# Kernel optimization log

Hardware: AMD Instinct MI355X
Metric: run time of the kernel (lower is better)

Reference implementation:

```python
import jax, jax.numpy as jnp
import numpy as np

N_NODES = 50000
N_EDGES = 800000
N_GRAPHS = 500
IN_DIM = 128
HID = 96
OUT_DIM = 64


def _lin(k, fan_in, fan_out):
    return jax.random.normal(k, (fan_in, fan_out), jnp.float32) / np.float32(np.sqrt(fan_in))


def setup_inputs() -> dict:
    key = jax.random.key(0)
    ks = jax.random.split(key, 12)
    x = jax.random.normal(ks[0], (N_NODES, IN_DIM), jnp.float32)
    edge_index = jax.random.randint(ks[1], (2, N_EDGES), 0, N_NODES)
    batch = jnp.sort(jax.random.randint(ks[2], (N_NODES,), 0, N_GRAPHS))
    return {
        "x": x,
        "edge_index": edge_index,
        "batch": batch,
        # GCN conv weights (first: in->hid, rest: hid->hid)
        "W0": _lin(ks[3], IN_DIM, HID), "b0": jnp.zeros((HID,), jnp.float32),
        "W1": _lin(ks[4], HID, HID),    "b1": jnp.zeros((HID,), jnp.float32),
        "W2": _lin(ks[5], HID, HID),    "b2": jnp.zeros((HID,), jnp.float32),
        # jumping-knowledge 'cat' projection: 3*hid -> hid
        "Wjk": _lin(ks[6], 3 * HID, HID), "bjk": jnp.zeros((HID,), jnp.float32),
        # fc_o MLP: hid -> hid -> out
        "Wm1": _lin(ks[7], HID, HID),   "bm1": jnp.zeros((HID,), jnp.float32),
        "Wm2": _lin(ks[8], HID, OUT_DIM), "bm2": jnp.zeros((OUT_DIM,), jnp.float32),
    }


def reference(x, edge_index, batch, W0, b0, W1, b1, W2, b2, Wjk, bjk, Wm1, bm1, Wm2, bm2):
    n = x.shape[0]
    loop = jnp.arange(n, dtype=edge_index.dtype)
    src = jnp.concatenate([edge_index[0], loop])  # [E+N] with self-loops
    dst = jnp.concatenate([edge_index[1], loop])
    # symmetric GCN normalization: D^{-1/2} (A+I) D^{-1/2}
    deg = jax.ops.segment_sum(jnp.ones_like(dst, x.dtype), dst, num_segments=n)
    dinv = jax.lax.rsqrt(jnp.maximum(deg, 1.0))  # deg >= 1 with self-loops
    norm = dinv[src] * dinv[dst]  # [E+N]

    def gcn_conv(h, W, b):
        m = (h @ W)[src] * norm[:, None]                      # gather + scale
        return jax.ops.segment_sum(m, dst, num_segments=n) + b  # scatter-add

    h1 = jax.nn.relu(gcn_conv(x, W0, b0))
    h2 = jax.nn.relu(gcn_conv(h1, W1, b1))
    h3 = jax.nn.relu(gcn_conv(h2, W2, b2))
    # JK 'cat' + final linear (PyG BasicGNN lin)
    h = jnp.concatenate([h1, h2, h3], axis=-1) @ Wjk + bjk    # [N, HID]
    # global add pooling over graphs
    emb_o = jax.ops.segment_sum(h, batch, num_segments=N_GRAPHS)  # [G, HID]
    # fc_o MLP (eval: dropout/identity-batchnorm omitted)
    pred_o = jax.nn.relu(emb_o @ Wm1 + bm1) @ Wm2 + bm2       # [G, OUT]
    return pred_o
```

## Files before the change

kernel.cpp:

```cpp
#include <hip/hip_runtime.h>
#include <hip/hip_fp16.h>

#define NN 50000
#define NE 800000
#define NG 500
#define IND 128
#define HD 96
#define OD 64

#define SCAN_CHUNK 2048
#define SCAN_BLOCKS ((NN + SCAN_CHUNK - 1) / SCAN_CHUNK)


__global__ void zero_k(int* __restrict__ cnt) {
  int i = blockIdx.x * 256 + threadIdx.x;
  if (i < NN) cnt[i] = 0;
}

__global__ void hist_k(const int* __restrict__ dst, int* __restrict__ cnt,
                       int* __restrict__ rank) {
  int i0 = (blockIdx.x * 256 + threadIdx.x) * 8;
  if (i0 + 8 <= NE) {
    int4 d0 = *reinterpret_cast<const int4*>(&dst[i0]);
    int4 d1 = *reinterpret_cast<const int4*>(&dst[i0 + 4]);
    int4 r0, r1;
    r0.x = atomicAdd(&cnt[d0.x], 1);
    r0.y = atomicAdd(&cnt[d0.y], 1);
    r0.z = atomicAdd(&cnt[d0.z], 1);
    r0.w = atomicAdd(&cnt[d0.w], 1);
    r1.x = atomicAdd(&cnt[d1.x], 1);
    r1.y = atomicAdd(&cnt[d1.y], 1);
    r1.z = atomicAdd(&cnt[d1.z], 1);
    r1.w = atomicAdd(&cnt[d1.w], 1);
    *reinterpret_cast<int4*>(&rank[i0]) = r0;
    *reinterpret_cast<int4*>(&rank[i0 + 4]) = r1;
  } else {
    for (int i = i0; i < NE; i++) rank[i] = atomicAdd(&cnt[dst[i]], 1);
  }
}

__global__ void gstart_k(const int* __restrict__ batch, int* __restrict__ gstart) {
  int n = blockIdx.x * 256 + threadIdx.x;
  if (n >= NN) return;
  if (n == 0) {
    for (int g = 0; g <= batch[0]; g++) gstart[g] = 0;
    for (int g = batch[NN - 1] + 1; g <= NG; g++) gstart[g] = NN;
  } else {
    int b0 = batch[n - 1], b1 = batch[n];
    for (int g = b0 + 1; g <= b1; g++) gstart[g] = n;
  }
}

__global__ __launch_bounds__(256) void scan_part_k(const int* __restrict__ cnt,
                                                   int* __restrict__ bsum,
                                                   float* __restrict__ dinv) {
  __shared__ int ts[256];
  const int tid = threadIdx.x;
  const int base = blockIdx.x * SCAN_CHUNK + tid * 8;
  int s = 0;
#pragma unroll
  for (int j = 0; j < 8; j++) {
    int idx = base + j;
    if (idx < NN) {
      int c = cnt[idx];
      s += c;
      dinv[idx] = rsqrtf((float)(c + 1));
    }
  }
  ts[tid] = s;
  __syncthreads();
  for (int off = 128; off > 0; off >>= 1) {
    if (tid < off) ts[tid] += ts[tid + off];
    __syncthreads();
  }
  if (tid == 0) bsum[blockIdx.x] = ts[0];
}

__global__ __launch_bounds__(64) void scan_top_k(const int* __restrict__ bsum,
                                                 int* __restrict__ boff,
                                                 int* __restrict__ row_ptr) {
  int tid = threadIdx.x;
  int v = (tid < SCAN_BLOCKS) ? bsum[tid] : 0;
  for (int off = 1; off < 64; off <<= 1) {
    int u = __shfl_up(v, off);
    if (tid >= off) v += u;
  }
  if (tid < SCAN_BLOCKS) boff[tid] = v - bsum[tid];
  if (tid == 0) row_ptr[NN] = NE;
}

__global__ __launch_bounds__(256) void scan_fin_k(const int* __restrict__ cnt,
                                                  const int* __restrict__ boff,
                                                  int* __restrict__ row_ptr) {
  __shared__ int ts[256];
  const int tid = threadIdx.x;
  const int base = blockIdx.x * SCAN_CHUNK + tid * 8;
  int v[8];
  int s = 0;
#pragma unroll
  for (int j = 0; j < 8; j++) {
    int idx = base + j;
    v[j] = (idx < NN) ? cnt[idx] : 0;
    s += v[j];
  }
  ts[tid] = s;
  __syncthreads();
  for (int off = 1; off < 256; off <<= 1) {
    int t = (tid >= off) ? ts[tid - off] : 0;
    __syncthreads();
    ts[tid] += t;
    __syncthreads();
  }
  int run = ((tid == 0) ? 0 : ts[tid - 1]) + boff[blockIdx.x];
#pragma unroll
  for (int j = 0; j < 8; j++) {
    int idx = base + j;
    if (idx < NN) row_ptr[idx] = run;
    run += v[j];
  }
}

__global__ void fill_k(const int* __restrict__ src, const int* __restrict__ dst,
                       const int* __restrict__ row_ptr, const int* __restrict__ rank,
                       int* __restrict__ col) {
  int i0 = (blockIdx.x * 256 + threadIdx.x) * 8;
  if (i0 + 8 <= NE) {
    int4 d0 = *reinterpret_cast<const int4*>(&dst[i0]);
    int4 d1 = *reinterpret_cast<const int4*>(&dst[i0 + 4]);
    int4 s0 = *reinterpret_cast<const int4*>(&src[i0]);
    int4 s1 = *reinterpret_cast<const int4*>(&src[i0 + 4]);
    int4 r0 = *reinterpret_cast<const int4*>(&rank[i0]);
    int4 r1 = *reinterpret_cast<const int4*>(&rank[i0 + 4]);
    int p0 = row_ptr[d0.x], p1 = row_ptr[d0.y], p2 = row_ptr[d0.z], p3 = row_ptr[d0.w];
    int p4 = row_ptr[d1.x], p5 = row_ptr[d1.y], p6 = row_ptr[d1.z], p7 = row_ptr[d1.w];
    col[p0 + r0.x] = s0.x * (HD * 2);
    col[p1 + r0.y] = s0.y * (HD * 2);
    col[p2 + r0.z] = s0.z * (HD * 2);
    col[p3 + r0.w] = s0.w * (HD * 2);
    col[p4 + r1.x] = s1.x * (HD * 2);
    col[p5 + r1.y] = s1.y * (HD * 2);
    col[p6 + r1.z] = s1.z * (HD * 2);
    col[p7 + r1.w] = s1.w * (HD * 2);
  } else {
    for (int i = i0; i < NE; i++)
      col[row_ptr[dst[i]] + rank[i]] = src[i] * (HD * 2);
  }
}

template <int K>
__global__ __launch_bounds__(256) void gemm_scale_k(const float* __restrict__ h,
                                                    const float* __restrict__ W,
                                                    const float* __restrict__ dinv,
                                                    __half* __restrict__ g) {
  __shared__ float hsT[32][66];
  __shared__ __attribute__((aligned(16))) float ws[32][100];
  const int tid = threadIdx.x;
  const int rowg = tid >> 3;
  const int colg = tid & 7;
  const int row0 = blockIdx.x * 64;

  float acc[2][12];
#pragma unroll
  for (int i = 0; i < 2; i++)
#pragma unroll
    for (int j = 0; j < 12; j++) acc[i][j] = 0.f;

  for (int k0 = 0; k0 < K; k0 += 32) {
#pragma unroll
    for (int lin = tid; lin < 512; lin += 256) {
      int r = lin >> 3, q = lin & 7;
      int grow = row0 + r;
      float4 v = make_float4(0.f, 0.f, 0.f, 0.f);
      if (grow < NN) v = *reinterpret_cast<const float4*>(&h[(long)grow * K + k0 + 4 * q]);
      hsT[4 * q + 0][r] = v.x;
      hsT[4 * q + 1][r] = v.y;
      hsT[4 * q + 2][r] = v.z;
      hsT[4 * q + 3][r] = v.w;
    }
#pragma unroll
    for (int lin = tid; lin < 768; lin += 256) {
      int kk = lin / 24, c4 = lin - kk * 24;
      *reinterpret_cast<float4*>(&ws[kk][4 * c4]) =
          *reinterpret_cast<const float4*>(&W[(long)(k0 + kk) * HD + 4 * c4]);
    }
    __syncthreads();
#pragma unroll 8
    for (int k = 0; k < 32; k++) {
      float2 a = *reinterpret_cast<const float2*>(&hsT[k][2 * rowg]);
      float4 w0 = *reinterpret_cast<const float4*>(&ws[k][12 * colg]);
      float4 w1 = *reinterpret_cast<const float4*>(&ws[k][12 * colg + 4]);
      float4 w2 = *reinterpret_cast<const float4*>(&ws[k][12 * colg + 8]);
      float wv[12] = {w0.x, w0.y, w0.z, w0.w, w1.x, w1.y, w1.z, w1.w,
                      w2.x, w2.y, w2.z, w2.w};
      float av[2] = {a.x, a.y};
#pragma unroll
      for (int i = 0; i < 2; i++)
#pragma unroll
        for (int j = 0; j < 12; j++) acc[i][j] = fmaf(av[i], wv[j], acc[i][j]);
    }
    __syncthreads();
  }
#pragma unroll
  for (int i = 0; i < 2; i++) {
    int row = row0 + 2 * rowg + i;
    if (row < NN) {
      float dv = dinv[row];
      __half2 hh[6];
#pragma unroll
      for (int q = 0; q < 6; q++)
        hh[q] = __floats2half2_rn(acc[i][2 * q] * dv, acc[i][2 * q + 1] * dv);
      __half* go = g + (long)row * HD + 12 * colg;
      *reinterpret_cast<float2*>(go) = *reinterpret_cast<float2*>(&hh[0]);
      *reinterpret_cast<float2*>(go + 4) = *reinterpret_cast<float2*>(&hh[2]);
      *reinterpret_cast<float2*>(go + 8) = *reinterpret_cast<float2*>(&hh[4]);
    }
  }
}

__global__ __launch_bounds__(256) void gather_k(const __half* __restrict__ g,
                                                const int* __restrict__ row_ptr,
                                                const int* __restrict__ col,
                                                const float* __restrict__ dinv,
                                                const float* __restrict__ bias,
                                                float* __restrict__ hout) {
  int d = blockIdx.x * 4 + (threadIdx.x >> 6);
  int lane = threadIdx.x & 63;
  if (d >= NN) return;
  const int cl = (lane < 48) ? lane : 0;
  const char* gb = reinterpret_cast<const char*>(g);
  const __half2* gd = reinterpret_cast<const __half2*>(gb + (long)d * (HD * 2));
  float2 fs = __half22float2(gd[cl]);
  float accx = fs.x, accy = fs.y;
  int e = row_ptr[d];
  const int end = row_ptr[d + 1];
  while (e < end) {
    int cnt = end - e; if (cnt > 64) cnt = 64;
    int cid = (lane < cnt) ? col[e + lane] : 0;
    int j = 0;
    for (; j + 16 <= cnt; j += 16) {
      const __half2* p0  = reinterpret_cast<const __half2*>(gb + (long)__shfl(cid, j + 0));
      const __half2* p1  = reinterpret_cast<const __half2*>(gb + (long)__shfl(cid, j + 1));
      const __half2* p2  = reinterpret_cast<const __half2*>(gb + (long)__shfl(cid, j + 2));
      const __half2* p3  = reinterpret_cast<const __half2*>(gb + (long)__shfl(cid, j + 3));
      const __half2* p4  = reinterpret_cast<const __half2*>(gb + (long)__shfl(cid, j + 4));
      const __half2* p5  = reinterpret_cast<const __half2*>(gb + (long)__shfl(cid, j + 5));
      const __half2* p6  = reinterpret_cast<const __half2*>(gb + (long)__shfl(cid, j + 6));
      const __half2* p7  = reinterpret_cast<const __half2*>(gb + (long)__shfl(cid, j + 7));
      const __half2* p8  = reinterpret_cast<const __half2*>(gb + (long)__shfl(cid, j + 8));
      const __half2* p9  = reinterpret_cast<const __half2*>(gb + (long)__shfl(cid, j + 9));
      const __half2* p10 = reinterpret_cast<const __half2*>(gb + (long)__shfl(cid, j + 10));
      const __half2* p11 = reinterpret_cast<const __half2*>(gb + (long)__shfl(cid, j + 11));
      const __half2* p12 = reinterpret_cast<const __half2*>(gb + (long)__shfl(cid, j + 12));
      const __half2* p13 = reinterpret_cast<const __half2*>(gb + (long)__shfl(cid, j + 13));
      const __half2* p14 = reinterpret_cast<const __half2*>(gb + (long)__shfl(cid, j + 14));
      const __half2* p15 = reinterpret_cast<const __half2*>(gb + (long)__shfl(cid, j + 15));
      __half2 v0 = p0[cl],  v1 = p1[cl],  v2 = p2[cl],  v3 = p3[cl];
      __half2 v4 = p4[cl],  v5 = p5[cl],  v6 = p6[cl],  v7 = p7[cl];
      __half2 v8 = p8[cl],  v9 = p9[cl],  v10 = p10[cl], v11 = p11[cl];
      __half2 v12 = p12[cl], v13 = p13[cl], v14 = p14[cl], v15 = p15[cl];
      float2 f;
      f = __half22float2(v0);  accx += f.x; accy += f.y;
      f = __half22float2(v1);  accx += f.x; accy += f.y;
      f = __half22float2(v2);  accx += f.x; accy += f.y;
      f = __half22float2(v3);  accx += f.x; accy += f.y;
      f = __half22float2(v4);  accx += f.x; accy += f.y;
      f = __half22float2(v5);  accx += f.x; accy += f.y;
      f = __half22float2(v6);  accx += f.x; accy += f.y;
      f = __half22float2(v7);  accx += f.x; accy += f.y;
      f = __half22float2(v8);  accx += f.x; accy += f.y;
      f = __half22float2(v9);  accx += f.x; accy += f.y;
      f = __half22float2(v10); accx += f.x; accy += f.y;
      f = __half22float2(v11); accx += f.x; accy += f.y;
      f = __half22float2(v12); accx += f.x; accy += f.y;
      f = __half22float2(v13); accx += f.x; accy += f.y;
      f = __half22float2(v14); accx += f.x; accy += f.y;
      f = __half22float2(v15); accx += f.x; accy += f.y;
    }
    for (; j + 8 <= cnt; j += 8) {
      const __half2* q0 = reinterpret_cast<const __half2*>(gb + (long)__shfl(cid, j + 0));
      const __half2* q1 = reinterpret_cast<const __half2*>(gb + (long)__shfl(cid, j + 1));
      const __half2* q2 = reinterpret_cast<const __half2*>(gb + (long)__shfl(cid, j + 2));
      const __half2* q3 = reinterpret_cast<const __half2*>(gb + (long)__shfl(cid, j + 3));
      const __half2* q4 = reinterpret_cast<const __half2*>(gb + (long)__shfl(cid, j + 4));
      const __half2* q5 = reinterpret_cast<const __half2*>(gb + (long)__shfl(cid, j + 5));
      const __half2* q6 = reinterpret_cast<const __half2*>(gb + (long)__shfl(cid, j + 6));
      const __half2* q7 = reinterpret_cast<const __half2*>(gb + (long)__shfl(cid, j + 7));
      __half2 v0 = q0[cl], v1 = q1[cl], v2 = q2[cl], v3 = q3[cl];
      __half2 v4 = q4[cl], v5 = q5[cl], v6 = q6[cl], v7 = q7[cl];
      float2 f;
      f = __half22float2(v0); accx += f.x; accy += f.y;
      f = __half22float2(v1); accx += f.x; accy += f.y;
      f = __half22float2(v2); accx += f.x; accy += f.y;
      f = __half22float2(v3); accx += f.x; accy += f.y;
      f = __half22float2(v4); accx += f.x; accy += f.y;
      f = __half22float2(v5); accx += f.x; accy += f.y;
      f = __half22float2(v6); accx += f.x; accy += f.y;
      f = __half22float2(v7); accx += f.x; accy += f.y;
    }
    for (; j < cnt; j++) {
      const __half2* p = reinterpret_cast<const __half2*>(gb + (long)__shfl(cid, j));
      float2 f = __half22float2(p[cl]);
      accx += f.x; accy += f.y;
    }
    e += 64;
  }
  if (lane < 48) {
    float dv = dinv[d];
    float2 bb = *reinterpret_cast<const float2*>(&bias[2 * lane]);
    float v0 = fmaxf(fmaf(accx, dv, bb.x), 0.f);
    float v1 = fmaxf(fmaf(accy, dv, bb.y), 0.f);
    *reinterpret_cast<float2*>(&hout[(long)d * HD + 2 * lane]) = make_float2(v0, v1);
  }
}

__global__ __launch_bounds__(256) void pool3_k(const float* __restrict__ hA,
                                               const float* __restrict__ hB,
                                               const float* __restrict__ hC,
                                               const int* __restrict__ gstart,
                                               float* __restrict__ P) {
  __shared__ float red[240][12];
  const int g = blockIdx.x;
  const int t = threadIdx.x;
  const int q = t % 24, s = t / 24;
  const int n0 = gstart[g], n1 = gstart[g + 1];
  if (t < 240) {
    float4 aA = make_float4(0.f, 0.f, 0.f, 0.f), aB = aA, aC = aA;
    for (int n = n0 + s; n < n1; n += 10) {
      float4 v;
      v = *reinterpret_cast<const float4*>(&hA[(long)n * HD + 4 * q]);
      aA.x += v.x; aA.y += v.y; aA.z += v.z; aA.w += v.w;
      v = *reinterpret_cast<const float4*>(&hB[(long)n * HD + 4 * q]);
      aB.x += v.x; aB.y += v.y; aB.z += v.z; aB.w += v.w;
      v = *reinterpret_cast<const float4*>(&hC[(long)n * HD + 4 * q]);
      aC.x += v.x; aC.y += v.y; aC.z += v.z; aC.w += v.w;
    }
    red[t][0] = aA.x; red[t][1] = aA.y; red[t][2]  = aA.z; red[t][3]  = aA.w;
    red[t][4] = aB.x; red[t][5] = aB.y; red[t][6]  = aB.z; red[t][7]  = aB.w;
    red[t][8] = aC.x; red[t][9] = aC.y; red[t][10] = aC.z; red[t][11] = aC.w;
  }
  __syncthreads();
  if (t < 24) {
    float sum[12];
#pragma unroll
    for (int c = 0; c < 12; c++) sum[c] = 0.f;
    for (int ss = 0; ss < 10; ss++)
#pragma unroll
      for (int c = 0; c < 12; c++) sum[c] += red[ss * 24 + t][c];
#pragma unroll
    for (int k = 0; k < 4; k++) {
      P[0 * NG * HD + g * HD + 4 * t + k] = sum[k];
      P[1 * NG * HD + g * HD + 4 * t + k] = sum[4 + k];
      P[2 * NG * HD + g * HD + 4 * t + k] = sum[8 + k];
    }
  }
}


__global__ void emb_k(const float* __restrict__ P, const int* __restrict__ gstart,
                      const float* __restrict__ Wjk, const float* __restrict__ bjk,
                      float* __restrict__ emb) {
  int idx = blockIdx.x * 256 + threadIdx.x;
  if (idx >= NG * HD) return;
  int gr = idx / HD, c = idx - gr * HD;
  const float* p1 = P + (long)gr * HD;
  const float* p2 = p1 + (long)NG * HD;
  const float* p3 = p2 + (long)NG * HD;
  float acc = (float)(gstart[gr + 1] - gstart[gr]) * bjk[c];
  for (int k = 0; k < HD; k++) {
    acc = fmaf(p1[k], Wjk[k * HD + c], acc);
    acc = fmaf(p2[k], Wjk[(HD + k) * HD + c], acc);
    acc = fmaf(p3[k], Wjk[(2 * HD + k) * HD + c], acc);
  }
  emb[idx] = acc;
}

__global__ void mlp1_k(const float* __restrict__ emb, const float* __restrict__ W,
                       const float* __restrict__ b, float* __restrict__ hid) {
  int idx = blockIdx.x * 256 + threadIdx.x;
  if (idx >= NG * HD) return;
  int gr = idx / HD, c = idx - gr * HD;
  const float* e = emb + (long)gr * HD;
  float acc = b[c];
  for (int k = 0; k < HD; k++) acc = fmaf(e[k], W[k * HD + c], acc);
  hid[idx] = fmaxf(acc, 0.f);
}

__global__ void mlp2_k(const float* __restrict__ hid, const float* __restrict__ W,
                       const float* __restrict__ b, float* __restrict__ out) {
  int idx = blockIdx.x * 256 + threadIdx.x;
  if (idx >= NG * OD) return;
  int gr = idx / OD, c = idx - gr * OD;
  const float* h = hid + (long)gr * HD;
  float acc = b[c];
  for (int k = 0; k < HD; k++) acc = fmaf(h[k], W[k * OD + c], acc);
  out[idx] = acc;
}


extern "C" void kernel_launch(void* const* d_in, const int* in_sizes, int n_in,
                              void* d_out, int out_size, void* d_ws, size_t ws_size,
                              hipStream_t stream) {
  const float* x = (const float*)d_in[0];
  const int* ei = (const int*)d_in[1];
  const int* batch = (const int*)d_in[2];
  const float* W0 = (const float*)d_in[3];  const float* b0 = (const float*)d_in[4];
  const float* W1 = (const float*)d_in[5];  const float* b1 = (const float*)d_in[6];
  const float* W2 = (const float*)d_in[7];  const float* b2 = (const float*)d_in[8];
  const float* Wjk = (const float*)d_in[9]; const float* bjk = (const float*)d_in[10];
  const float* Wm1 = (const float*)d_in[11]; const float* bm1 = (const float*)d_in[12];
  const float* Wm2 = (const float*)d_in[13]; const float* bm2 = (const float*)d_in[14];
  const int* srcp = ei;
  const int* dstp = ei + NE;

  char* wp = (char*)d_ws;
  size_t off = 0;
  auto alloc = [&](size_t bytes) -> void* {
    void* p = wp + off;
    off += bytes;
    off = (off + 255) & ~(size_t)255;
    return p;
  };
  int* cnt    = (int*)alloc((size_t)NN * 4);
  int* rowp   = (int*)alloc((size_t)(NN + 1) * 4);
  int* rank   = (int*)alloc((size_t)NE * 4);
  int* colb   = (int*)alloc((size_t)NE * 4);
  float* dinv = (float*)alloc((size_t)NN * 4);
  int* gstart = (int*)alloc((size_t)(NG + 1) * 4);
  int* bsum   = (int*)alloc((size_t)SCAN_BLOCKS * 4);
  int* boff   = (int*)alloc((size_t)SCAN_BLOCKS * 4);
  __half* g   = (__half*)alloc((size_t)NN * HD * 2);
  float* hA   = (float*)alloc((size_t)NN * HD * 4);
  float* hB   = (float*)alloc((size_t)NN * HD * 4);
  float* hC   = (float*)alloc((size_t)NN * HD * 4);
  float* P    = (float*)alloc((size_t)3 * NG * HD * 4);
  float* emb  = (float*)alloc((size_t)NG * HD * 4);
  float* hid  = (float*)alloc((size_t)NG * HD * 4);

  zero_k<<<(NN + 255) / 256, 256, 0, stream>>>(cnt);

  const int eb8 = (NE / 8 + 255) / 256;
  hist_k<<<eb8, 256, 0, stream>>>(dstp, cnt, rank);
  gstart_k<<<(NN + 255) / 256, 256, 0, stream>>>(batch, gstart);
  scan_part_k<<<SCAN_BLOCKS, 256, 0, stream>>>(cnt, bsum, dinv);
  scan_top_k<<<1, 64, 0, stream>>>(bsum, boff, rowp);
  scan_fin_k<<<SCAN_BLOCKS, 256, 0, stream>>>(cnt, boff, rowp);
  fill_k<<<eb8, 256, 0, stream>>>(srcp, dstp, rowp, rank, colb);

  const int gemm_grid = (NN + 63) / 64;
  const int gath_grid = (NN + 3) / 4;
  gemm_scale_k<IND><<<gemm_grid, 256, 0, stream>>>(x, W0, dinv, g);
  gather_k<<<gath_grid, 256, 0, stream>>>(g, rowp, colb, dinv, b0, hA);
  gemm_scale_k<HD><<<gemm_grid, 256, 0, stream>>>(hA, W1, dinv, g);
  gather_k<<<gath_grid, 256, 0, stream>>>(g, rowp, colb, dinv, b1, hB);
  gemm_scale_k<HD><<<gemm_grid, 256, 0, stream>>>(hB, W2, dinv, g);
  gather_k<<<gath_grid, 256, 0, stream>>>(g, rowp, colb, dinv, b2, hC);

  pool3_k<<<NG, 256, 0, stream>>>(hA, hB, hC, gstart, P);

  emb_k<<<(NG * HD + 255) / 256, 256, 0, stream>>>(P, gstart, Wjk, bjk, emb);
  mlp1_k<<<(NG * HD + 255) / 256, 256, 0, stream>>>(emb, Wm1, bm1, hid);
  mlp2_k<<<(NG * OD + 255) / 256, 256, 0, stream>>>(hid, Wm2, bm2, (float*)d_out);
}
```

Measured before the change: 262.4 us.

## Store hidden activations in fp16 and gather four neighbors per wavefront step

Hidden layer outputs hA/hB/hC are now stored as fp16 instead of fp32. The next GEMM and the pooling kernel read them at half the bytes and convert to float on load. The gather kernel is restructured so each wavefront processes four neighbor rows at once, with 12 lanes per row loading 16 bytes each. The partial sums are then reduced with shuffles. This cuts activation traffic and raises bytes per load, at the cost of fp16 rounding of intermediate activations and an extra cross-lane reduction.

```diff
diff --git a/kernel.cpp b/kernel.cpp
--- a/kernel.cpp
+++ b/kernel.cpp
@@ -147,8 +147,8 @@
   }
 }
 
-template <int K>
-__global__ __launch_bounds__(256) void gemm_scale_k(const float* __restrict__ h,
+template <int K, typename T>
+__global__ __launch_bounds__(256) void gemm_scale_k(const T* __restrict__ h,
                                                     const float* __restrict__ W,
                                                     const float* __restrict__ dinv,
                                                     __half* __restrict__ g) {
@@ -166,16 +166,38 @@
     for (int j = 0; j < 12; j++) acc[i][j] = 0.f;
 
   for (int k0 = 0; k0 < K; k0 += 32) {
-#pragma unroll
-    for (int lin = tid; lin < 512; lin += 256) {
-      int r = lin >> 3, q = lin & 7;
-      int grow = row0 + r;
-      float4 v = make_float4(0.f, 0.f, 0.f, 0.f);
-      if (grow < NN) v = *reinterpret_cast<const float4*>(&h[(long)grow * K + k0 + 4 * q]);
-      hsT[4 * q + 0][r] = v.x;
-      hsT[4 * q + 1][r] = v.y;
-      hsT[4 * q + 2][r] = v.z;
-      hsT[4 * q + 3][r] = v.w;
+    if constexpr (sizeof(T) == 4) {
+#pragma unroll
+      for (int lin = tid; lin < 512; lin += 256) {
+        int r = lin >> 3, q = lin & 7;
+        int grow = row0 + r;
+        float4 v = make_float4(0.f, 0.f, 0.f, 0.f);
+        if (grow < NN)
+          v = *reinterpret_cast<const float4*>(&h[(long)grow * K + k0 + 4 * q]);
+        hsT[4 * q + 0][r] = v.x;
+        hsT[4 * q + 1][r] = v.y;
+        hsT[4 * q + 2][r] = v.z;
+        hsT[4 * q + 3][r] = v.w;
+      }
+    } else {
+      {
+        int r = tid >> 2, q = tid & 3;
+        int grow = row0 + r;
+        if (grow < NN) {
+          int4 raw = *reinterpret_cast<const int4*>(
+              reinterpret_cast<const __half*>(h) + (long)grow * K + k0 + 8 * q);
+          const __half2* hp = reinterpret_cast<const __half2*>(&raw);
+#pragma unroll
+          for (int t = 0; t < 4; t++) {
+            float2 f = __half22float2(hp[t]);
+            hsT[8 * q + 2 * t + 0][r] = f.x;
+            hsT[8 * q + 2 * t + 1][r] = f.y;
+          }
+        } else {
+#pragma unroll
+          for (int t = 0; t < 8; t++) hsT[8 * q + t][r] = 0.f;
+        }
+      }
     }
 #pragma unroll
     for (int lin = tid; lin < 768; lin += 256) {
@@ -222,100 +244,102 @@
                                                 const int* __restrict__ col,
                                                 const float* __restrict__ dinv,
                                                 const float* __restrict__ bias,
-                                                float* __restrict__ hout) {
+                                                __half* __restrict__ hout) {
   int d = blockIdx.x * 4 + (threadIdx.x >> 6);
   int lane = threadIdx.x & 63;
   if (d >= NN) return;
-  const int cl = (lane < 48) ? lane : 0;
+  const bool active = (lane < 48);
+  const int s = active ? (lane / 12) : 0;
+  const int c = active ? (lane % 12) : 0;
+  const int cofs = 16 * c;
   const char* gb = reinterpret_cast<const char*>(g);
-  const __half2* gd = reinterpret_cast<const __half2*>(gb + (long)d * (HD * 2));
-  float2 fs = __half22float2(gd[cl]);
-  float accx = fs.x, accy = fs.y;
+  const int own = d * (HD * 2);
+
+  float acc[8];
+#pragma unroll
+  for (int k = 0; k < 8; k++) acc[k] = 0.f;
+
+  {
+    float4 raw = *reinterpret_cast<const float4*>(gb + own + cofs);
+    const __half2* hp = reinterpret_cast<const __half2*>(&raw);
+    float m = (active && s == 0) ? 1.f : 0.f;
+#pragma unroll
+    for (int q = 0; q < 4; q++) {
+      float2 f = __half22float2(hp[q]);
+      acc[2 * q + 0] = fmaf(m, f.x, acc[2 * q + 0]);
+      acc[2 * q + 1] = fmaf(m, f.y, acc[2 * q + 1]);
+    }
+  }
+
   int e = row_ptr[d];
   const int end = row_ptr[d + 1];
   while (e < end) {
     int cnt = end - e; if (cnt > 64) cnt = 64;
-    int cid = (lane < cnt) ? col[e + lane] : 0;
+    int cid = (lane < cnt) ? col[e + lane] : own;
     int j = 0;
     for (; j + 16 <= cnt; j += 16) {
-      const __half2* p0  = reinterpret_cast<const __half2*>(gb + (long)__shfl(cid, j + 0));
-      const __half2* p1  = reinterpret_cast<const __half2*>(gb + (long)__shfl(cid, j + 1));
-      const __half2* p2  = reinterpret_cast<const __half2*>(gb + (long)__shfl(cid, j + 2));
-      const __half2* p3  = reinterpret_cast<const __half2*>(gb + (long)__shfl(cid, j + 3));
-      const __half2* p4  = reinterpret_cast<const __half2*>(gb + (long)__shfl(cid, j + 4));
-      const __half2* p5  = reinterpret_cast<const __half2*>(gb + (long)__shfl(cid, j + 5));
-      const __half2* p6  = reinterpret_cast<const __half2*>(gb + (long)__shfl(cid, j + 6));
-      const __half2* p7  = reinterpret_cast<const __half2*>(gb + (long)__shfl(cid, j + 7));
-      const __half2* p8  = reinterpret_cast<const __half2*>(gb + (long)__shfl(cid, j + 8));
-      const __half2* p9  = reinterpret_cast<const __half2*>(gb + (long)__shfl(cid, j + 9));
-      const __half2* p10 = reinterpret_cast<const __half2*>(gb + (long)__shfl(cid, j + 10));
-      const __half2* p11 = reinterpret_cast<const __half2*>(gb + (long)__shfl(cid, j + 11));
-      const __half2* p12 = reinterpret_cast<const __half2*>(gb + (long)__shfl(cid, j + 12));
-      const __half2* p13 = reinterpret_cast<const __half2*>(gb + (long)__shfl(cid, j + 13));
-      const __half2* p14 = reinterpret_cast<const __half2*>(gb + (long)__shfl(cid, j + 14));
-      const __half2* p15 = reinterpret_cast<const __half2*>(gb + (long)__shfl(cid, j + 15));
-      __half2 v0 = p0[cl],  v1 = p1[cl],  v2 = p2[cl],  v3 = p3[cl];
-      __half2 v4 = p4[cl],  v5 = p5[cl],  v6 = p6[cl],  v7 = p7[cl];
-      __half2 v8 = p8[cl],  v9 = p9[cl],  v10 = p10[cl], v11 = p11[cl];
-      __half2 v12 = p12[cl], v13 = p13[cl], v14 = p14[cl], v15 = p15[cl];
-      float2 f;
-      f = __half22float2(v0);  accx += f.x; accy += f.y;
-      f = __half22float2(v1);  accx += f.x; accy += f.y;
-      f = __half22float2(v2);  accx += f.x; accy += f.y;
-      f = __half22float2(v3);  accx += f.x; accy += f.y;
-      f = __half22float2(v4);  accx += f.x; accy += f.y;
-      f = __half22float2(v5);  accx += f.x; accy += f.y;
-      f = __half22float2(v6);  accx += f.x; accy += f.y;
-      f = __half22float2(v7);  accx += f.x; accy += f.y;
-      f = __half22float2(v8);  accx += f.x; accy += f.y;
-      f = __half22float2(v9);  accx += f.x; accy += f.y;
-      f = __half22float2(v10); accx += f.x; accy += f.y;
-      f = __half22float2(v11); accx += f.x; accy += f.y;
-      f = __half22float2(v12); accx += f.x; accy += f.y;
-      f = __half22float2(v13); accx += f.x; accy += f.y;
-      f = __half22float2(v14); accx += f.x; accy += f.y;
-      f = __half22float2(v15); accx += f.x; accy += f.y;
-    }
-    for (; j + 8 <= cnt; j += 8) {
-      const __half2* q0 = reinterpret_cast<const __half2*>(gb + (long)__shfl(cid, j + 0));
-      const __half2* q1 = reinterpret_cast<const __half2*>(gb + (long)__shfl(cid, j + 1));
-      const __half2* q2 = reinterpret_cast<const __half2*>(gb + (long)__shfl(cid, j + 2));
-      const __half2* q3 = reinterpret_cast<const __half2*>(gb + (long)__shfl(cid, j + 3));
-      const __half2* q4 = reinterpret_cast<const __half2*>(gb + (long)__shfl(cid, j + 4));
-      const __half2* q5 = reinterpret_cast<const __half2*>(gb + (long)__shfl(cid, j + 5));
-      const __half2* q6 = reinterpret_cast<const __half2*>(gb + (long)__shfl(cid, j + 6));
-      const __half2* q7 = reinterpret_cast<const __half2*>(gb + (long)__shfl(cid, j + 7));
-      __half2 v0 = q0[cl], v1 = q1[cl], v2 = q2[cl], v3 = q3[cl];
-      __half2 v4 = q4[cl], v5 = q5[cl], v6 = q6[cl], v7 = q7[cl];
-      float2 f;
-      f = __half22float2(v0); accx += f.x; accy += f.y;
-      f = __half22float2(v1); accx += f.x; accy += f.y;
-      f = __half22float2(v2); accx += f.x; accy += f.y;
-      f = __half22float2(v3); accx += f.x; accy += f.y;
-      f = __half22float2(v4); accx += f.x; accy += f.y;
-      f = __half22float2(v5); accx += f.x; accy += f.y;
-      f = __half22float2(v6); accx += f.x; accy += f.y;
-      f = __half22float2(v7); accx += f.x; accy += f.y;
-    }
-    for (; j < cnt; j++) {
-      const __half2* p = reinterpret_cast<const __half2*>(gb + (long)__shfl(cid, j));
-      float2 f = __half22float2(p[cl]);
-      accx += f.x; accy += f.y;
+      int o0 = __shfl(cid, j + s);
+      int o1 = __shfl(cid, j + 4 + s);
+      int o2 = __shfl(cid, j + 8 + s);
+      int o3 = __shfl(cid, j + 12 + s);
+      float4 r0 = *reinterpret_cast<const float4*>(gb + o0 + cofs);
+      float4 r1 = *reinterpret_cast<const float4*>(gb + o1 + cofs);
+      float4 r2 = *reinterpret_cast<const float4*>(gb + o2 + cofs);
+      float4 r3 = *reinterpret_cast<const float4*>(gb + o3 + cofs);
+      const __half2* h0 = reinterpret_cast<const __half2*>(&r0);
+      const __half2* h1 = reinterpret_cast<const __half2*>(&r1);
+      const __half2* h2 = reinterpret_cast<const __half2*>(&r2);
+      const __half2* h3 = reinterpret_cast<const __half2*>(&r3);
+#pragma unroll
+      for (int q = 0; q < 4; q++) {
+        float2 f0 = __half22float2(h0[q]);
+        float2 f1 = __half22float2(h1[q]);
+        float2 f2 = __half22float2(h2[q]);
+        float2 f3 = __half22float2(h3[q]);
+        acc[2 * q + 0] += (f0.x + f1.x) + (f2.x + f3.x);
+        acc[2 * q + 1] += (f0.y + f1.y) + (f2.y + f3.y);
+      }
+    }
+    for (; j < cnt; j += 4) {
+      int o = __shfl(cid, j + s);
+      float m = (j + s < cnt) ? 1.f : 0.f;
+      float4 r = *reinterpret_cast<const float4*>(gb + o + cofs);
+      const __half2* hp = reinterpret_cast<const __half2*>(&r);
+#pragma unroll
+      for (int q = 0; q < 4; q++) {
+        float2 f = __half22float2(hp[q]);
+        acc[2 * q + 0] = fmaf(m, f.x, acc[2 * q + 0]);
+        acc[2 * q + 1] = fmaf(m, f.y, acc[2 * q + 1]);
+      }
     }
     e += 64;
   }
-  if (lane < 48) {
+
+#pragma unroll
+  for (int k = 0; k < 8; k++) acc[k] += __shfl(acc[k], lane + 24);
+#pragma unroll
+  for (int k = 0; k < 8; k++) acc[k] += __shfl(acc[k], lane + 12);
+
+  if (lane < 12) {
     float dv = dinv[d];
-    float2 bb = *reinterpret_cast<const float2*>(&bias[2 * lane]);
-    float v0 = fmaxf(fmaf(accx, dv, bb.x), 0.f);
-    float v1 = fmaxf(fmaf(accy, dv, bb.y), 0.f);
-    *reinterpret_cast<float2*>(&hout[(long)d * HD + 2 * lane]) = make_float2(v0, v1);
-  }
-}
-
-__global__ __launch_bounds__(256) void pool3_k(const float* __restrict__ hA,
-                                               const float* __restrict__ hB,
-                                               const float* __restrict__ hC,
+    float4 b0 = *reinterpret_cast<const float4*>(&bias[8 * c]);
+    float4 b1 = *reinterpret_cast<const float4*>(&bias[8 * c + 4]);
+    float vb[8] = {b0.x, b0.y, b0.z, b0.w, b1.x, b1.y, b1.z, b1.w};
+    __half2 hh[4];
+#pragma unroll
+    for (int q = 0; q < 4; q++) {
+      float v0 = fmaxf(fmaf(acc[2 * q + 0], dv, vb[2 * q + 0]), 0.f);
+      float v1 = fmaxf(fmaf(acc[2 * q + 1], dv, vb[2 * q + 1]), 0.f);
+      hh[q] = __floats2half2_rn(v0, v1);
+    }
+    *reinterpret_cast<float4*>(&hout[(long)d * HD + 8 * c]) =
+        *reinterpret_cast<float4*>(hh);
+  }
+}
+
+__global__ __launch_bounds__(256) void pool3_k(const __half* __restrict__ hA,
+                                               const __half* __restrict__ hB,
+                                               const __half* __restrict__ hC,
                                                const int* __restrict__ gstart,
                                                float* __restrict__ P) {
   __shared__ float red[240][12];
@@ -324,28 +348,40 @@
   const int q = t % 24, s = t / 24;
   const int n0 = gstart[g], n1 = gstart[g + 1];
   if (t < 240) {
-    float4 aA = make_float4(0.f, 0.f, 0.f, 0.f), aB = aA, aC = aA;
+    float aA[4] = {0.f, 0.f, 0.f, 0.f}, aB[4] = {0.f, 0.f, 0.f, 0.f},
+          aC[4] = {0.f, 0.f, 0.f, 0.f};
     for (int n = n0 + s; n < n1; n += 10) {
-      float4 v;
-      v = *reinterpret_cast<const float4*>(&hA[(long)n * HD + 4 * q]);
-      aA.x += v.x; aA.y += v.y; aA.z += v.z; aA.w += v.w;
-      v = *reinterpret_cast<const float4*>(&hB[(long)n * HD + 4 * q]);
-      aB.x += v.x; aB.y += v.y; aB.z += v.z; aB.w += v.w;
-      v = *reinterpret_cast<const float4*>(&hC[(long)n * HD + 4 * q]);
-      aC.x += v.x; aC.y += v.y; aC.z += v.z; aC.w += v.w;
-    }
-    red[t][0] = aA.x; red[t][1] = aA.y; red[t][2]  = aA.z; red[t][3]  = aA.w;
-    red[t][4] = aB.x; red[t][5] = aB.y; red[t][6]  = aB.z; red[t][7]  = aB.w;
-    red[t][8] = aC.x; red[t][9] = aC.y; red[t][10] = aC.z; red[t][11] = aC.w;
+      float2 rA = *reinterpret_cast<const float2*>(&hA[(long)n * HD + 4 * q]);
+      float2 rB = *reinterpret_cast<const float2*>(&hB[(long)n * HD + 4 * q]);
+      float2 rC = *reinterpret_cast<const float2*>(&hC[(long)n * HD + 4 * q]);
+      const __half2* pA = reinterpret_cast<const __half2*>(&rA);
+      const __half2* pB = reinterpret_cast<const __half2*>(&rB);
+      const __half2* pC = reinterpret_cast<const __half2*>(&rC);
+#pragma unroll
+      for (int u = 0; u < 2; u++) {
+        float2 fA = __half22float2(pA[u]);
+        float2 fB = __half22float2(pB[u]);
+        float2 fC = __half22float2(pC[u]);
+        aA[2 * u] += fA.x; aA[2 * u + 1] += fA.y;
+        aB[2 * u] += fB.x; aB[2 * u + 1] += fB.y;
+        aC[2 * u] += fC.x; aC[2 * u + 1] += fC.y;
+      }
+    }
+#pragma unroll
+    for (int u = 0; u < 4; u++) {
+      red[t][u] = aA[u];
+      red[t][4 + u] = aB[u];
+      red[t][8 + u] = aC[u];
+    }
   }
   __syncthreads();
   if (t < 24) {
     float sum[12];
 #pragma unroll
-    for (int c = 0; c < 12; c++) sum[c] = 0.f;
+    for (int u = 0; u < 12; u++) sum[u] = 0.f;
     for (int ss = 0; ss < 10; ss++)
 #pragma unroll
-      for (int c = 0; c < 12; c++) sum[c] += red[ss * 24 + t][c];
+      for (int u = 0; u < 12; u++) sum[u] += red[ss * 24 + t][u];
 #pragma unroll
     for (int k = 0; k < 4; k++) {
       P[0 * NG * HD + g * HD + 4 * t + k] = sum[k];
@@ -429,9 +465,9 @@
   int* bsum   = (int*)alloc((size_t)SCAN_BLOCKS * 4);
   int* boff   = (int*)alloc((size_t)SCAN_BLOCKS * 4);
   __half* g   = (__half*)alloc((size_t)NN * HD * 2);
-  float* hA   = (float*)alloc((size_t)NN * HD * 4);
-  float* hB   = (float*)alloc((size_t)NN * HD * 4);
-  float* hC   = (float*)alloc((size_t)NN * HD * 4);
+  __half* hA  = (__half*)alloc((size_t)NN * HD * 2);
+  __half* hB  = (__half*)alloc((size_t)NN * HD * 2);
+  __half* hC  = (__half*)alloc((size_t)NN * HD * 2);
   float* P    = (float*)alloc((size_t)3 * NG * HD * 4);
   float* emb  = (float*)alloc((size_t)NG * HD * 4);
   float* hid  = (float*)alloc((size_t)NG * HD * 4);
@@ -448,11 +484,11 @@
 
   const int gemm_grid = (NN + 63) / 64;
   const int gath_grid = (NN + 3) / 4;
-  gemm_scale_k<IND><<<gemm_grid, 256, 0, stream>>>(x, W0, dinv, g);
+  gemm_scale_k<IND, float><<<gemm_grid, 256, 0, stream>>>(x, W0, dinv, g);
   gather_k<<<gath_grid, 256, 0, stream>>>(g, rowp, colb, dinv, b0, hA);
-  gemm_scale_k<HD><<<gemm_grid, 256, 0, stream>>>(hA, W1, dinv, g);
+  gemm_scale_k<HD, __half><<<gemm_grid, 256, 0, stream>>>(hA, W1, dinv, g);
   gather_k<<<gath_grid, 256, 0, stream>>>(g, rowp, colb, dinv, b1, hB);
-  gemm_scale_k<HD><<<gemm_grid, 256, 0, stream>>>(hB, W2, dinv, g);
+  gemm_scale_k<HD, __half><<<gemm_grid, 256, 0, stream>>>(hB, W2, dinv, g);
   gather_k<<<gath_grid, 256, 0, stream>>>(g, rowp, colb, dinv, b2, hC);
 
   pool3_k<<<NG, 256, 0, stream>>>(hA, hB, hC, gstart, P);
```

After: 252.0 us. -3.9%, faster.
